# Optimization experiments

Hardware: AMD Instinct MI355X
Metric: run time of the kernel (lower is better)

## Reference

```python
import jax, jax.numpy as jnp
import numpy as np

LAPLACE_SCALE = 0.5


def setup_inputs() -> dict:
    key = jax.random.key(0)
    k1, k2, k3 = jax.random.split(key, 3)
    B, M, D = 8, 512, 64
    return {
        "k": jax.random.normal(k1, (B, M, D), dtype=jnp.float32),
        "v": jax.random.normal(k2, (B, M, D), dtype=jnp.float32),
        "q": jax.random.normal(k3, (B, M, D), dtype=jnp.float32),
    }


def reference(k, v, q):
    # Laplace attention branch (faithful to original, including comparing k to v):
    # k_: [B,1,M,D], v_: [B,M,1,D] -> unnorm: [B,M,M]
    unnorm = jnp.abs((k[:, None, :, :] - v[:, :, None, :]) * LAPLACE_SCALE).sum(axis=-1)
    weights = jax.nn.softmax(unnorm, axis=-1)  # [B,M,M]
    rep = jnp.einsum('bik,bkj->bij', weights, v)  # [B,M,D]
    return rep
```

## Files before the change

kernel.cpp:

```cpp
#include <hip/hip_runtime.h>


typedef _Float16 h2 __attribute__((ext_vector_type(2)));

#if __has_builtin(__builtin_amdgcn_fdot2)
#define FDOT2(a, b, c) __builtin_amdgcn_fdot2((a), (b), (c), false)
#else
static __device__ inline float FDOT2(h2 a, h2 b, float c) {
    return c + (float)a.x * (float)b.x + (float)a.y * (float)b.y;
}
#endif

#if __has_builtin(__builtin_amdgcn_sad_u16)
#define SADU16(a, b, c) __builtin_amdgcn_sad_u16((a), (b), (c))
#else
static __device__ inline unsigned SADU16(unsigned a, unsigned b, unsigned c) {
    const unsigned al = a & 0xFFFFu, ah = a >> 16;
    const unsigned bl = b & 0xFFFFu, bh = b >> 16;
    const unsigned dl = al > bl ? al - bl : bl - al;
    const unsigned dh = ah > bh ? ah - bh : bh - ah;
    return c + dl + dh;
}
#endif

static __device__ inline unsigned pk16(float x, float y) {
    h2 h;
    h.x = (_Float16)x;
    h.y = (_Float16)y;
    return __builtin_bit_cast(unsigned, h);
}

static __device__ inline unsigned q16(float x) {
    const float f = fminf(fmaxf(x * 4096.0f + 32768.5f, 0.5f), 65535.0f);
    return (unsigned)f;
}

constexpr int B_ = 8, M_ = 512, D_ = 64;
constexpr int GRID1 = 8 * 16 * 8;
constexpr size_t REP_ELEMS = (size_t)GRID1 * 2048;
#define C2L 1.761099911e-4f

constexpr int OFF_KH  = 0;
constexpr int OFF_VH  = 2176;
constexpr int OFF_VJ2 = 3328;
constexpr int OFF_WH  = 5504;
constexpr int OFF_MR  = 6656;
constexpr int OFF_DEN = 6784;
constexpr int LDS_U   = 6912;

__global__ __launch_bounds__(256, 4)
void laplace_k1(const float* __restrict__ K, const float* __restrict__ V,
                float* __restrict__ rep_part, float2* __restrict__ md_part) {
    __shared__ __align__(16) unsigned lds[LDS_U];

    const int blk = blockIdx.x;
    const int b  = blk >> 7;
    const int it = (blk >> 3) & 15;
    const int jg = blk & 7;
    const int i0 = it * 32, j0 = jg * 64;

    const float* __restrict__ Kb = K + (size_t)b * (M_ * D_);
    const float* __restrict__ Vb = V + (size_t)b * (M_ * D_);

    const int t = threadIdx.x;

    {
        const int row = t >> 2, dq = t & 3;
        const float* kp = Kb + (size_t)(j0 + row) * D_ + dq * 16;
#pragma unroll
        for (int c = 0; c < 4; ++c) {
            const float4 q = *reinterpret_cast<const float4*>(kp + 4 * c);
            lds[OFF_KH + (dq * 8 + 2 * c + 0) * 68 + row] = q16(q.x) | (q16(q.y) << 16);
            lds[OFF_KH + (dq * 8 + 2 * c + 1) * 68 + row] = q16(q.z) | (q16(q.w) << 16);
        }
    }
    {
        const int row = t >> 3, dq = t & 7;
        const float* vp = Vb + (size_t)(i0 + row) * D_ + dq * 8;
        const float4 a = *reinterpret_cast<const float4*>(vp);
        const float4 c4 = *reinterpret_cast<const float4*>(vp + 4);
        lds[OFF_VH + (dq * 4 + 0) * 36 + row] = q16(a.x)  | (q16(a.y)  << 16);
        lds[OFF_VH + (dq * 4 + 1) * 36 + row] = q16(a.z)  | (q16(a.w)  << 16);
        lds[OFF_VH + (dq * 4 + 2) * 36 + row] = q16(c4.x) | (q16(c4.y) << 16);
        lds[OFF_VH + (dq * 4 + 3) * 36 + row] = q16(c4.z) | (q16(c4.w) << 16);
    }
    {
        const int j2 = t >> 3;
        const int dc = (t & 7) * 8;
        const float* r0 = Vb + (size_t)(j0 + 2 * j2) * D_ + dc;
        const float* r1 = r0 + D_;
        unsigned o[8];
#pragma unroll
        for (int c = 0; c < 8; c += 4) {
            const float4 a = *reinterpret_cast<const float4*>(r0 + c);
            const float4 bq = *reinterpret_cast<const float4*>(r1 + c);
            o[c + 0] = pk16(a.x, bq.x);
            o[c + 1] = pk16(a.y, bq.y);
            o[c + 2] = pk16(a.z, bq.z);
            o[c + 3] = pk16(a.w, bq.w);
        }
        *reinterpret_cast<uint4*>(&lds[OFF_VJ2 + j2 * 68 + dc]) =
            make_uint4(o[0], o[1], o[2], o[3]);
        *reinterpret_cast<uint4*>(&lds[OFF_VJ2 + j2 * 68 + dc + 4]) =
            make_uint4(o[4], o[5], o[6], o[7]);
    }
    __syncthreads();

    const int wv = t >> 6, lane = t & 63;
    const int ig = lane >> 2;
    const int jq = lane & 3;

    unsigned sacc[2][4];
#pragma unroll
    for (int a = 0; a < 2; ++a)
#pragma unroll
        for (int c = 0; c < 4; ++c) sacc[a][c] = 0u;

    const unsigned* pV = lds + OFF_VH + ig * 2;
    const unsigned* pK = lds + OFF_KH + wv * 16 + jq * 4;

#pragma unroll 8
    for (int d2 = 0; d2 < 32; ++d2) {
        const uint2 va = *reinterpret_cast<const uint2*>(pV + d2 * 36);
        const uint4 ka = *reinterpret_cast<const uint4*>(pK + d2 * 68);
        sacc[0][0] = SADU16(ka.x, va.x, sacc[0][0]);
        sacc[0][1] = SADU16(ka.y, va.x, sacc[0][1]);
        sacc[0][2] = SADU16(ka.z, va.x, sacc[0][2]);
        sacc[0][3] = SADU16(ka.w, va.x, sacc[0][3]);
        sacc[1][0] = SADU16(ka.x, va.y, sacc[1][0]);
        sacc[1][1] = SADU16(ka.y, va.y, sacc[1][1]);
        sacc[1][2] = SADU16(ka.z, va.y, sacc[1][2]);
        sacc[1][3] = SADU16(ka.w, va.y, sacc[1][3]);
    }

    float sf[2][4];
#pragma unroll
    for (int a = 0; a < 2; ++a)
#pragma unroll
        for (int c = 0; c < 4; ++c) sf[a][c] = (float)sacc[a][c] * C2L;

    float rm[2];
#pragma unroll
    for (int a = 0; a < 2; ++a) {
        rm[a] = fmaxf(fmaxf(sf[a][0], sf[a][1]), fmaxf(sf[a][2], sf[a][3]));
        rm[a] = fmaxf(rm[a], __shfl_xor(rm[a], 1));
        rm[a] = fmaxf(rm[a], __shfl_xor(rm[a], 2));
    }
    float* mr = reinterpret_cast<float*>(lds + OFF_MR);
    float* dnl = reinterpret_cast<float*>(lds + OFF_DEN);
    if (jq == 0)
        *reinterpret_cast<float2*>(&mr[wv * 32 + ig * 2]) = make_float2(rm[0], rm[1]);
    __syncthreads();

    float m[2];
    {
        const float2 m0 = *reinterpret_cast<const float2*>(&mr[0 * 32 + ig * 2]);
        const float2 m1 = *reinterpret_cast<const float2*>(&mr[1 * 32 + ig * 2]);
        const float2 m2 = *reinterpret_cast<const float2*>(&mr[2 * 32 + ig * 2]);
        const float2 m3 = *reinterpret_cast<const float2*>(&mr[3 * 32 + ig * 2]);
        m[0] = fmaxf(fmaxf(m0.x, m1.x), fmaxf(m2.x, m3.x));
        m[1] = fmaxf(fmaxf(m0.y, m1.y), fmaxf(m2.y, m3.y));
    }

    float w[2][4], den[2];
#pragma unroll
    for (int a = 0; a < 2; ++a) {
        den[a] = 0.f;
#pragma unroll
        for (int c = 0; c < 4; ++c) {
            w[a][c] = exp2f(sf[a][c] - m[a]);
            den[a] += w[a][c];
        }
        den[a] += __shfl_xor(den[a], 1);
        den[a] += __shfl_xor(den[a], 2);
    }
    if (jq == 0)
        *reinterpret_cast<float2*>(&dnl[wv * 32 + ig * 2]) = make_float2(den[0], den[1]);

    {
        const int j2 = wv * 8 + jq * 2;
#pragma unroll
        for (int a = 0; a < 2; ++a) {
            lds[OFF_WH + (j2 + 0) * 36 + ig * 2 + a] = pk16(w[a][0], w[a][1]);
            lds[OFF_WH + (j2 + 1) * 36 + ig * 2 + a] = pk16(w[a][2], w[a][3]);
        }
    }
    __syncthreads();

    const int ig2 = lane >> 3;
    const int dg2 = lane & 7;

    float acc[4][2];
#pragma unroll
    for (int a = 0; a < 4; ++a) { acc[a][0] = 0.f; acc[a][1] = 0.f; }

    const unsigned* pW  = lds + OFF_WH + ig2 * 4;
    const unsigned* pVJ = lds + OFF_VJ2 + wv * 16 + dg2 * 2;

#pragma unroll 8
    for (int j2 = 0; j2 < 32; ++j2) {
        const uint4 wq = *reinterpret_cast<const uint4*>(pW + j2 * 36);
        const uint2 vq = *reinterpret_cast<const uint2*>(pVJ + j2 * 68);
        const h2 v0 = __builtin_bit_cast(h2, vq.x);
        const h2 v1 = __builtin_bit_cast(h2, vq.y);
        const unsigned wA[4] = {wq.x, wq.y, wq.z, wq.w};
#pragma unroll
        for (int a = 0; a < 4; ++a) {
            const h2 wa = __builtin_bit_cast(h2, wA[a]);
            acc[a][0] = FDOT2(wa, v0, acc[a][0]);
            acc[a][1] = FDOT2(wa, v1, acc[a][1]);
        }
    }

    float* rp = rep_part + (size_t)blk * 2048;
#pragma unroll
    for (int a = 0; a < 4; ++a)
        *reinterpret_cast<float2*>(&rp[(ig2 * 4 + a) * 64 + wv * 16 + dg2 * 2]) =
            make_float2(acc[a][0], acc[a][1]);

    if (t < 32) {
        const float mf = fmaxf(fmaxf(mr[t], mr[32 + t]), fmaxf(mr[64 + t], mr[96 + t]));
        const float df = (dnl[t] + dnl[32 + t]) + (dnl[64 + t] + dnl[96 + t]);
        md_part[(size_t)blk * 32 + t] = make_float2(mf, df);
    }
}

__global__ __launch_bounds__(256)
void laplace_k2(const float* __restrict__ rep_part,
                const float2* __restrict__ md_part,
                float* __restrict__ out) {
    const int gid = blockIdx.x * 256 + threadIdx.x;
    const int b   = gid >> 15;
    const int i   = (gid >> 6) & 511;
    const int dd  = gid & 63;
    const int it  = i >> 5, il = i & 31;

    const size_t base = (size_t)(b * 16 + it) * 8;

    float2 md[8];
#pragma unroll
    for (int jt = 0; jt < 8; ++jt) md[jt] = md_part[(base + jt) * 32 + il];

    float M = md[0].x;
#pragma unroll
    for (int jt = 1; jt < 8; ++jt) M = fmaxf(M, md[jt].x);

    float acc = 0.f, dsum = 0.f;
    const float* rp = rep_part + base * 2048 + (size_t)il * 64 + dd;
#pragma unroll
    for (int jt = 0; jt < 8; ++jt) {
        const float f = exp2f(md[jt].x - M);
        dsum += f * md[jt].y;
        acc  += f * rp[(size_t)jt * 2048];
    }
    out[gid] = acc / dsum;
}

extern "C" void kernel_launch(void* const* d_in, const int* in_sizes, int n_in,
                              void* d_out, int out_size, void* d_ws, size_t ws_size,
                              hipStream_t stream) {
    const float* K = (const float*)d_in[0];
    const float* V = (const float*)d_in[1];
    float* out      = (float*)d_out;
    float* rep_part = (float*)d_ws;
    float2* md_part = (float2*)(rep_part + REP_ELEMS);

    laplace_k1<<<dim3(GRID1), dim3(256), 0, stream>>>(K, V, rep_part, md_part);
    laplace_k2<<<dim3((B_ * M_ * D_) / 256), dim3(256), 0, stream>>>(
        rep_part, md_part, out);
}
```

Baseline: 20.18 us.

## Retile score phase into 4x4 register tiles with split-D reduction and per-half softmax partials

The score phase now gives each thread a 4x4 (i,j) register tile and splits the D dimension across wave pairs. Partial SAD sums are combined through a new LDS scratch area, and the full softmax runs only in half the waves, with each j-half writing its own max/denominator partial straight to global memory. The PV phase likewise uses 4x4 tiles split by j-half, which doubles the partial slots and makes the second kernel merge 16 partials instead of 8. The q16 clamp is also dropped. The aim is fewer LDS loads per SAD/dot operation and fewer block-wide softmax reductions, at the cost of extra LDS, idle waves during softmax, and more global partial traffic.

```diff
diff --git a/kernel.cpp b/kernel.cpp
--- a/kernel.cpp
+++ b/kernel.cpp
@@ -31,22 +31,21 @@
 }
 
 static __device__ inline unsigned q16(float x) {
-    const float f = fminf(fmaxf(x * 4096.0f + 32768.5f, 0.5f), 65535.0f);
-    return (unsigned)f;
+    return (unsigned)(x * 4096.0f + 32768.5f);
 }
 
 constexpr int B_ = 8, M_ = 512, D_ = 64;
 constexpr int GRID1 = 8 * 16 * 8;
-constexpr size_t REP_ELEMS = (size_t)GRID1 * 2048;
+constexpr int NSLOT = GRID1 * 2;
+constexpr size_t REP_ELEMS = (size_t)NSLOT * 2048;
 #define C2L 1.761099911e-4f
 
 constexpr int OFF_KH  = 0;
 constexpr int OFF_VH  = 2176;
 constexpr int OFF_VJ2 = 3328;
 constexpr int OFF_WH  = 5504;
-constexpr int OFF_MR  = 6656;
-constexpr int OFF_DEN = 6784;
-constexpr int LDS_U   = 6912;
+constexpr int OFF_SC  = 6656;
+constexpr int LDS_U   = 8704;
 
 __global__ __launch_bounds__(256, 4)
 void laplace_k1(const float* __restrict__ K, const float* __restrict__ V,
@@ -54,10 +53,10 @@
     __shared__ __align__(16) unsigned lds[LDS_U];
 
     const int blk = blockIdx.x;
-    const int b  = blk >> 7;
-    const int it = (blk >> 3) & 15;
-    const int jg = blk & 7;
-    const int i0 = it * 32, j0 = jg * 64;
+    const int b   = blk >> 7;
+    const int it  = (blk >> 3) & 15;
+    const int jgB = blk & 7;
+    const int i0 = it * 32, j0 = jgB * 64;
 
     const float* __restrict__ Kb = K + (size_t)b * (M_ * D_);
     const float* __restrict__ Vb = V + (size_t)b * (M_ * D_);
@@ -77,7 +76,7 @@
     {
         const int row = t >> 3, dq = t & 7;
         const float* vp = Vb + (size_t)(i0 + row) * D_ + dq * 8;
-        const float4 a = *reinterpret_cast<const float4*>(vp);
+        const float4 a  = *reinterpret_cast<const float4*>(vp);
         const float4 c4 = *reinterpret_cast<const float4*>(vp + 4);
         lds[OFF_VH + (dq * 4 + 0) * 36 + row] = q16(a.x)  | (q16(a.y)  << 16);
         lds[OFF_VH + (dq * 4 + 1) * 36 + row] = q16(a.z)  | (q16(a.w)  << 16);
@@ -92,7 +91,7 @@
         unsigned o[8];
 #pragma unroll
         for (int c = 0; c < 8; c += 4) {
-            const float4 a = *reinterpret_cast<const float4*>(r0 + c);
+            const float4 a  = *reinterpret_cast<const float4*>(r0 + c);
             const float4 bq = *reinterpret_cast<const float4*>(r1 + c);
             o[c + 0] = pk16(a.x, bq.x);
             o[c + 1] = pk16(a.y, bq.y);
@@ -107,122 +106,125 @@
     __syncthreads();
 
     const int wv = t >> 6, lane = t & 63;
-    const int ig = lane >> 2;
-    const int jq = lane & 3;
-
-    unsigned sacc[2][4];
-#pragma unroll
-    for (int a = 0; a < 2; ++a)
+    const int jh = wv & 1;
+    const int dh = wv >> 1;
+    const int ig = lane >> 3;
+    const int jg = lane & 7;
+
+    unsigned sacc[4][4];
+#pragma unroll
+    for (int a = 0; a < 4; ++a)
 #pragma unroll
         for (int c = 0; c < 4; ++c) sacc[a][c] = 0u;
 
-    const unsigned* pV = lds + OFF_VH + ig * 2;
-    const unsigned* pK = lds + OFF_KH + wv * 16 + jq * 4;
+    const unsigned* pV = lds + OFF_VH + dh * (16 * 36) + ig * 4;
+    const unsigned* pK = lds + OFF_KH + dh * (16 * 68) + jh * 32 + jg * 4;
 
 #pragma unroll 8
-    for (int d2 = 0; d2 < 32; ++d2) {
-        const uint2 va = *reinterpret_cast<const uint2*>(pV + d2 * 36);
+    for (int d2 = 0; d2 < 16; ++d2) {
+        const uint4 va = *reinterpret_cast<const uint4*>(pV + d2 * 36);
         const uint4 ka = *reinterpret_cast<const uint4*>(pK + d2 * 68);
-        sacc[0][0] = SADU16(ka.x, va.x, sacc[0][0]);
-        sacc[0][1] = SADU16(ka.y, va.x, sacc[0][1]);
-        sacc[0][2] = SADU16(ka.z, va.x, sacc[0][2]);
-        sacc[0][3] = SADU16(ka.w, va.x, sacc[0][3]);
-        sacc[1][0] = SADU16(ka.x, va.y, sacc[1][0]);
-        sacc[1][1] = SADU16(ka.y, va.y, sacc[1][1]);
-        sacc[1][2] = SADU16(ka.z, va.y, sacc[1][2]);
-        sacc[1][3] = SADU16(ka.w, va.y, sacc[1][3]);
-    }
-
-    float sf[2][4];
-#pragma unroll
-    for (int a = 0; a < 2; ++a)
-#pragma unroll
-        for (int c = 0; c < 4; ++c) sf[a][c] = (float)sacc[a][c] * C2L;
-
-    float rm[2];
-#pragma unroll
-    for (int a = 0; a < 2; ++a) {
-        rm[a] = fmaxf(fmaxf(sf[a][0], sf[a][1]), fmaxf(sf[a][2], sf[a][3]));
-        rm[a] = fmaxf(rm[a], __shfl_xor(rm[a], 1));
-        rm[a] = fmaxf(rm[a], __shfl_xor(rm[a], 2));
-    }
-    float* mr = reinterpret_cast<float*>(lds + OFF_MR);
-    float* dnl = reinterpret_cast<float*>(lds + OFF_DEN);
-    if (jq == 0)
-        *reinterpret_cast<float2*>(&mr[wv * 32 + ig * 2]) = make_float2(rm[0], rm[1]);
+        const unsigned vaA[4] = {va.x, va.y, va.z, va.w};
+        const unsigned kaA[4] = {ka.x, ka.y, ka.z, ka.w};
+#pragma unroll
+        for (int a = 0; a < 4; ++a)
+#pragma unroll
+            for (int c = 0; c < 4; ++c)
+                sacc[a][c] = SADU16(kaA[c], vaA[a], sacc[a][c]);
+    }
+
+    uint4* sc = reinterpret_cast<uint4*>(lds + OFF_SC);
+    if (dh == 1) {
+        const int col = jh * 64 + lane;
+#pragma unroll
+        for (int a = 0; a < 4; ++a)
+            sc[a * 128 + col] =
+                make_uint4(sacc[a][0], sacc[a][1], sacc[a][2], sacc[a][3]);
+    }
     __syncthreads();
 
-    float m[2];
-    {
-        const float2 m0 = *reinterpret_cast<const float2*>(&mr[0 * 32 + ig * 2]);
-        const float2 m1 = *reinterpret_cast<const float2*>(&mr[1 * 32 + ig * 2]);
-        const float2 m2 = *reinterpret_cast<const float2*>(&mr[2 * 32 + ig * 2]);
-        const float2 m3 = *reinterpret_cast<const float2*>(&mr[3 * 32 + ig * 2]);
-        m[0] = fmaxf(fmaxf(m0.x, m1.x), fmaxf(m2.x, m3.x));
-        m[1] = fmaxf(fmaxf(m0.y, m1.y), fmaxf(m2.y, m3.y));
-    }
-
-    float w[2][4], den[2];
-#pragma unroll
-    for (int a = 0; a < 2; ++a) {
-        den[a] = 0.f;
-#pragma unroll
-        for (int c = 0; c < 4; ++c) {
-            w[a][c] = exp2f(sf[a][c] - m[a]);
-            den[a] += w[a][c];
-        }
-        den[a] += __shfl_xor(den[a], 1);
-        den[a] += __shfl_xor(den[a], 2);
-    }
-    if (jq == 0)
-        *reinterpret_cast<float2*>(&dnl[wv * 32 + ig * 2]) = make_float2(den[0], den[1]);
-
-    {
-        const int j2 = wv * 8 + jq * 2;
-#pragma unroll
-        for (int a = 0; a < 2; ++a) {
-            lds[OFF_WH + (j2 + 0) * 36 + ig * 2 + a] = pk16(w[a][0], w[a][1]);
-            lds[OFF_WH + (j2 + 1) * 36 + ig * 2 + a] = pk16(w[a][2], w[a][3]);
+    if (dh == 0) {
+        const int col = jh * 64 + lane;
+#pragma unroll
+        for (int a = 0; a < 4; ++a) {
+            const uint4 q = sc[a * 128 + col];
+            sacc[a][0] += q.x; sacc[a][1] += q.y;
+            sacc[a][2] += q.z; sacc[a][3] += q.w;
+        }
+        float sf[4][4];
+#pragma unroll
+        for (int a = 0; a < 4; ++a)
+#pragma unroll
+            for (int c = 0; c < 4; ++c) sf[a][c] = (float)sacc[a][c] * C2L;
+
+        float rm[4];
+#pragma unroll
+        for (int a = 0; a < 4; ++a) {
+            rm[a] = fmaxf(fmaxf(sf[a][0], sf[a][1]), fmaxf(sf[a][2], sf[a][3]));
+            rm[a] = fmaxf(rm[a], __shfl_xor(rm[a], 1));
+            rm[a] = fmaxf(rm[a], __shfl_xor(rm[a], 2));
+            rm[a] = fmaxf(rm[a], __shfl_xor(rm[a], 4));
+        }
+        float w[4][4], den[4];
+#pragma unroll
+        for (int a = 0; a < 4; ++a) {
+            den[a] = 0.f;
+#pragma unroll
+            for (int c = 0; c < 4; ++c) {
+                w[a][c] = exp2f(sf[a][c] - rm[a]);
+                den[a] += w[a][c];
+            }
+            den[a] += __shfl_xor(den[a], 1);
+            den[a] += __shfl_xor(den[a], 2);
+            den[a] += __shfl_xor(den[a], 4);
+        }
+        const int j2b = jh * 16 + jg * 2;
+        *reinterpret_cast<uint4*>(&lds[OFF_WH + (j2b + 0) * 36 + ig * 4]) =
+            make_uint4(pk16(w[0][0], w[0][1]), pk16(w[1][0], w[1][1]),
+                       pk16(w[2][0], w[2][1]), pk16(w[3][0], w[3][1]));
+        *reinterpret_cast<uint4*>(&lds[OFF_WH + (j2b + 1) * 36 + ig * 4]) =
+            make_uint4(pk16(w[0][2], w[0][3]), pk16(w[1][2], w[1][3]),
+                       pk16(w[2][2], w[2][3]), pk16(w[3][2], w[3][3]));
+        if (jg == 0) {
+            float* mp = reinterpret_cast<float*>(md_part + (size_t)(blk * 2 + jh) * 32 + ig * 4);
+            *reinterpret_cast<float4*>(mp)     = make_float4(rm[0], den[0], rm[1], den[1]);
+            *reinterpret_cast<float4*>(mp + 4) = make_float4(rm[2], den[2], rm[3], den[3]);
         }
     }
     __syncthreads();
 
     const int ig2 = lane >> 3;
-    const int dg2 = lane & 7;
-
-    float acc[4][2];
-#pragma unroll
-    for (int a = 0; a < 4; ++a) { acc[a][0] = 0.f; acc[a][1] = 0.f; }
-
-    const unsigned* pW  = lds + OFF_WH + ig2 * 4;
-    const unsigned* pVJ = lds + OFF_VJ2 + wv * 16 + dg2 * 2;
+    const int dg  = lane & 7;
+
+    float acc[4][4];
+#pragma unroll
+    for (int a = 0; a < 4; ++a)
+#pragma unroll
+        for (int c = 0; c < 4; ++c) acc[a][c] = 0.f;
+
+    const unsigned* pW  = lds + OFF_WH + jh * (16 * 36) + ig2 * 4;
+    const unsigned* pVJ = lds + OFF_VJ2 + jh * (16 * 68) + dh * 32 + dg * 4;
 
 #pragma unroll 8
-    for (int j2 = 0; j2 < 32; ++j2) {
+    for (int j2 = 0; j2 < 16; ++j2) {
         const uint4 wq = *reinterpret_cast<const uint4*>(pW + j2 * 36);
-        const uint2 vq = *reinterpret_cast<const uint2*>(pVJ + j2 * 68);
-        const h2 v0 = __builtin_bit_cast(h2, vq.x);
-        const h2 v1 = __builtin_bit_cast(h2, vq.y);
+        const uint4 vq = *reinterpret_cast<const uint4*>(pVJ + j2 * 68);
         const unsigned wA[4] = {wq.x, wq.y, wq.z, wq.w};
+        const unsigned vA[4] = {vq.x, vq.y, vq.z, vq.w};
 #pragma unroll
         for (int a = 0; a < 4; ++a) {
             const h2 wa = __builtin_bit_cast(h2, wA[a]);
-            acc[a][0] = FDOT2(wa, v0, acc[a][0]);
-            acc[a][1] = FDOT2(wa, v1, acc[a][1]);
-        }
-    }
-
-    float* rp = rep_part + (size_t)blk * 2048;
+#pragma unroll
+            for (int c = 0; c < 4; ++c)
+                acc[a][c] = FDOT2(wa, __builtin_bit_cast(h2, vA[c]), acc[a][c]);
+        }
+    }
+
+    float* rp = rep_part + (size_t)(blk * 2 + jh) * 2048;
 #pragma unroll
     for (int a = 0; a < 4; ++a)
-        *reinterpret_cast<float2*>(&rp[(ig2 * 4 + a) * 64 + wv * 16 + dg2 * 2]) =
-            make_float2(acc[a][0], acc[a][1]);
-
-    if (t < 32) {
-        const float mf = fmaxf(fmaxf(mr[t], mr[32 + t]), fmaxf(mr[64 + t], mr[96 + t]));
-        const float df = (dnl[t] + dnl[32 + t]) + (dnl[64 + t] + dnl[96 + t]);
-        md_part[(size_t)blk * 32 + t] = make_float2(mf, df);
-    }
+        *reinterpret_cast<float4*>(&rp[(ig2 * 4 + a) * 64 + dh * 32 + dg * 4]) =
+            make_float4(acc[a][0], acc[a][1], acc[a][2], acc[a][3]);
 }
 
 __global__ __launch_bounds__(256)
@@ -235,23 +237,23 @@
     const int dd  = gid & 63;
     const int it  = i >> 5, il = i & 31;
 
-    const size_t base = (size_t)(b * 16 + it) * 8;
-
-    float2 md[8];
-#pragma unroll
-    for (int jt = 0; jt < 8; ++jt) md[jt] = md_part[(base + jt) * 32 + il];
+    const size_t base = (size_t)(b * 16 + it) * 16;
+
+    float2 md[16];
+#pragma unroll
+    for (int s = 0; s < 16; ++s) md[s] = md_part[(base + s) * 32 + il];
 
     float M = md[0].x;
 #pragma unroll
-    for (int jt = 1; jt < 8; ++jt) M = fmaxf(M, md[jt].x);
+    for (int s = 1; s < 16; ++s) M = fmaxf(M, md[s].x);
 
     float acc = 0.f, dsum = 0.f;
     const float* rp = rep_part + base * 2048 + (size_t)il * 64 + dd;
 #pragma unroll
-    for (int jt = 0; jt < 8; ++jt) {
-        const float f = exp2f(md[jt].x - M);
-        dsum += f * md[jt].y;
-        acc  += f * rp[(size_t)jt * 2048];
+    for (int s = 0; s < 16; ++s) {
+        const float f = exp2f(md[s].x - M);
+        dsum += f * md[s].y;
+        acc  += f * rp[(size_t)s * 2048];
     }
     out[gid] = acc / dsum;
 }
```

Result: slower. 25.49 us (+26.3%).
